# Kernel optimization log

Hardware: AMD Instinct MI355X
Metric: run time of the kernel (lower is better)

Reference implementation:

```python
import jax, jax.numpy as jnp
import numpy as np
from jax import lax

N, CIN, COUT, T, V, G, K = 32, 64, 64, 256, 25, 8, 3  # batch, channels, time, joints, groups, subsets
EPS = 1e-5  # BatchNorm eps


def setup_inputs() -> dict:
    key = jax.random.key(0)
    ks = jax.random.split(key, 10)
    x = jax.random.normal(ks[0], (N, CIN, T, V), jnp.float32)
    # DecoupleA param: A reshaped [3,1,V,V] tiled over groups (torch .repeat tiles)
    A0 = jax.random.uniform(ks[1], (K, 1, V, V), jnp.float32)
    DecoupleA = jnp.tile(A0, (1, G, 1, 1))
    W = jax.random.normal(ks[2], (CIN, COUT * K), jnp.float32) * np.float32(np.sqrt(0.5 / (COUT * K)))
    b = jnp.full((1, COUT * K, 1, 1), 1e-6, jnp.float32)
    g0 = 1.0 + 0.1 * jax.random.normal(ks[3], (COUT * K,), jnp.float32)
    b0 = 0.1 * jax.random.normal(ks[4], (COUT * K,), jnp.float32)
    g1 = 1.0 + 0.1 * jax.random.normal(ks[5], (COUT,), jnp.float32)
    b1 = 0.1 * jax.random.normal(ks[6], (COUT,), jnp.float32)
    conv_w = jax.random.normal(ks[7], (COUT, COUT, 9, 1), jnp.float32) * np.float32(np.sqrt(2.0 / (COUT * 9)))
    conv_b = jnp.zeros((COUT,), jnp.float32)
    g2 = 1.0 + 0.1 * jax.random.normal(ks[8], (COUT,), jnp.float32)
    b2 = 0.1 * jax.random.normal(ks[9], (COUT,), jnp.float32)
    return {"x": x, "DecoupleA": DecoupleA, "W": W, "b": b, "g0": g0, "b0": b0,
            "g1": g1, "b1": b1, "conv_w": conv_w, "conv_b": conv_b, "g2": g2, "b2": b2,
            "keep_prob": 1}


def _bn_eval(y, g, be):
    # inference BN with running_mean=0, running_var=1
    return y * (g / jnp.sqrt(1.0 + EPS))[None, :, None, None] + be[None, :, None, None]


def reference(x, DecoupleA, W, b, g0, b0, g1, b1, conv_w, conv_b, g2, b2, keep_prob):
    # ---- unit_gcn ----
    learn_A = jnp.tile(DecoupleA, (1, COUT // G, 1, 1))           # [3, COUT, V, V]
    # norm(): right-multiply by diag((colsum + 0.001)^-1) == scale columns
    invD = 1.0 / (jnp.sum(learn_A, axis=2) + 0.001)               # [3, COUT, V]
    normA = learn_A * invD[:, :, None, :]
    y = jnp.einsum('nctw,cd->ndtw', x, W) + b                     # [N, 3*COUT, T, V]
    y = _bn_eval(y, g0, b0)
    y = y.reshape(N, K, COUT, T, V)
    y = jnp.einsum('nkctv,kcvw->nctw', y, normA)                  # message passing
    y = _bn_eval(y, g1, b1)
    y = jax.nn.relu(y + x)                                        # down = identity (CIN==COUT)
    # ---- unit_tcn (keep_prob==1 -> DropBlocks are identity) ----
    z = lax.conv_general_dilated(y, conv_w, (1, 1), [(4, 4), (0, 0)],
                                 dimension_numbers=('NCHW', 'OIHW', 'NCHW'))
    z = z + conv_b[None, :, None, None]
    z = _bn_eval(z, g2, b2)
    # ---- residual (identity, CIN==COUT, stride=1; skip-DropBlocks identity) ----
    return jax.nn.relu(z + x)
```

## Files before the change

### kernel.cpp

```cpp
#include <hip/hip_runtime.h>
#include <hip/hip_bf16.h>
#include <stdint.h>


typedef const float* fp;
typedef __attribute__((ext_vector_type(8))) short short8;
typedef __attribute__((ext_vector_type(4))) float floatx4;

__device__ __forceinline__ float us2f(unsigned int u){
  union { unsigned int i; float f; } c; c.i = u << 16; return c.f;
}
__device__ __forceinline__ unsigned short f2us(float f){
  __hip_bfloat16 h = __float2bfloat16(f);
  return *reinterpret_cast<unsigned short*>(&h);
}
__device__ __forceinline__ void gload_lds16(const void* g, void* l){
  __builtin_amdgcn_global_load_lds(
      (const __attribute__((address_space(1))) void*)g,
      (__attribute__((address_space(3))) void*)l, 16, 0, 0);
}


__global__ __launch_bounds__(256) void k_prep(
    fp x, fp A, fp W, fp b, fp g0, fp b0, fp g1, fp b1,
    fp cw, fp cb, fp g2, fp b2,
    unsigned short* U, float* biasU, unsigned short* xb,
    float* cbe, unsigned short* cwetb)
{
  int bid = blockIdx.x, tid = threadIdx.x;
  const float inv_s = rsqrtf(1.0f + 1e-5f);
  __shared__ __align__(16) char smemraw[26624];

  if (bid < 1792) {
    int m = bid;
    if (m >= 1600) {
      for (int k = tid; k < 1600; k += 256) U[(long long)m*1600 + k] = 0;
      return;
    }
    float* nAL   = (float*)smemraw;
    float* WeffL = (float*)(smemraw + 512);
    float* cs3   = (float*)(smemraw + 1408);
    int c = m & 63, w = m >> 6, g = c & 7;
    if (tid < 75) {
      int kk = tid / 25, vv = tid % 25;
      nAL[tid] = A[((kk*8 + g)*25 + vv)*25 + w];
    }
    if (tid < 192) {
      int kk = tid >> 6, cin = tid & 63;
      WeffL[tid] = W[cin*192 + kk*64 + c] * (g0[kk*64 + c] * inv_s);
    }
    __syncthreads();
    if (tid < 3) {
      float s = 0.f;
      for (int vv = 0; vv < 25; vv++) s += nAL[tid*25 + vv];
      cs3[tid] = s + 0.001f;
    }
    __syncthreads();
    if (tid < 75) nAL[tid] = nAL[tid] / cs3[tid/25];
    __syncthreads();
    float s1 = g1[c] * inv_s;
    for (int k = tid; k < 1600; k += 256) {
      int cin = k / 25, vv = k - cin*25;
      float acc = WeffL[cin]       * nAL[vv]
                + WeffL[64 + cin]  * nAL[25 + vv]
                + WeffL[128 + cin] * nAL[50 + vv];
      acc *= s1;
      if (cin == c && vv == w) acc += 1.0f;
      U[(long long)m*1600 + k] = f2us(acc);
    }
    if (tid == 0) {
      float acc = 0.f;
      for (int kk = 0; kk < 3; kk++) {
        int d = kk*64 + c;
        float be = b[d] * (g0[d] * inv_s) + b0[d];
        for (int v = 0; v < 25; v++) acc += be * nAL[kk*25 + v];
      }
      biasU[m] = acc * s1 + b1[c];
    }
    return;
  }

  if (bid < 2816) {
    int bxt = bid - 1792;
    int n = bxt >> 5, tb = bxt & 31, t0 = tb*8;
    unsigned short* xs = (unsigned short*)smemraw;
    for (int e = tid; e < 12800; e += 256) {
      int c = e / 200, r = e - c*200, tt = r / 25, v = r - tt*25;
      xs[(c*8 + tt)*26 + v] = f2us(x[((n*64 + c)*256 + t0 + tt)*25 + v]);
    }
    __syncthreads();
    for (int e4 = tid; e4 < 3200; e4 += 256) {
      int base = e4 * 4;
      int tt = base / 1600, q0 = base - tt*1600;
      int c = q0 / 25, v = q0 - c*25;
      ushort4 pk;
      pk.x = xs[(c*8 + tt)*26 + v]; if (++v == 25){v = 0; c++;}
      pk.y = xs[(c*8 + tt)*26 + v]; if (++v == 25){v = 0; c++;}
      pk.z = xs[(c*8 + tt)*26 + v]; if (++v == 25){v = 0; c++;}
      pk.w = xs[(c*8 + tt)*26 + v];
      *(ushort4*)(xb + (long long)(n*256 + t0 + tt)*1600 + q0) = pk;
    }
    return;
  }

  int gid = (bid - 2816)*256 + tid;
  if (gid < 36864) {
    int o = gid / 576, r = gid % 576;
    int j = r / 64, i = r % 64;
    cwetb[gid] = f2us(cw[(o*64+i)*9 + j] * (g2[o] * inv_s));
    return;
  }
  gid -= 36864;
  if (gid < 64) {
    cbe[gid] = cb[gid] * (g2[gid] * inv_s) + b2[gid];
  }
}

__global__ __launch_bounds__(256, 2) void k_gemm(
    const unsigned short* U, const unsigned short* xb, const float* biasU,
    unsigned short* yb)
{
  int bm = blockIdx.x >> 6, bn = blockIdx.x & 63;
  int n = bn >> 1, t0 = (bn & 1) * 128;
  int tid = threadIdx.x, lane = tid & 63, wid = tid >> 6;
  int l15 = lane & 15, grp = lane >> 4;

  __shared__ __align__(16) unsigned short As[256*64];
  __shared__ __align__(16) unsigned short Bs[128*64];

  const unsigned short* gA[8];
  const unsigned short* gB[4];
  unsigned short* lA[8];
  unsigned short* lB[4];
  #pragma unroll
  for (int it = 0; it < 8; it++) {
    int e = it*256 + tid;
    int row = e >> 3, li = e & 7;
    int kcol = (li ^ (row & 7)) * 8;
    gA[it] = U + (long long)(bm*256 + row)*1600 + kcol;
    lA[it] = As + e*8;
  }
  #pragma unroll
  for (int it = 0; it < 4; it++) {
    int e = it*256 + tid;
    int row = e >> 3, li = e & 7;
    int kcol = (li ^ (row & 7)) * 8;
    gB[it] = xb + (long long)(n*256 + t0 + row)*1600 + kcol;
    lB[it] = Bs + e*8;
  }

  floatx4 acc[4][8];
  #pragma unroll
  for (int i = 0; i < 4; i++)
    #pragma unroll
    for (int j = 0; j < 8; j++) acc[i][j] = (floatx4){0.f,0.f,0.f,0.f};

  for (int kc = 0; kc < 25; kc++) {
    #pragma unroll
    for (int it = 0; it < 8; it++) gload_lds16(gA[it] + kc*64, lA[it]);
    #pragma unroll
    for (int it = 0; it < 4; it++) gload_lds16(gB[it] + kc*64, lB[it]);
    __syncthreads();
    #pragma unroll
    for (int ks = 0; ks < 2; ks++) {
      int colk = ((ks*4 + grp) ^ (l15 & 7)) * 8;
      short8 af[4], bf[8];
      #pragma unroll
      for (int i = 0; i < 4; i++)
        af[i] = *(const short8*)(As + (wid*64 + i*16 + l15)*64 + colk);
      #pragma unroll
      for (int j = 0; j < 8; j++)
        bf[j] = *(const short8*)(Bs + (j*16 + l15)*64 + colk);
      #pragma unroll
      for (int i = 0; i < 4; i++)
        #pragma unroll
        for (int j = 0; j < 8; j++)
          acc[i][j] = __builtin_amdgcn_mfma_f32_16x16x32_bf16(af[i], bf[j], acc[i][j], 0, 0, 0);
    }
    __syncthreads();
  }

  #pragma unroll
  for (int i = 0; i < 4; i++) {
    int mbase = bm*256 + wid*64 + i*16 + grp*4;
    if (mbase >= 1600) continue;
    float4 bu = *(const float4*)(biasU + mbase);
    #pragma unroll
    for (int j = 0; j < 8; j++) {
      int col = j*16 + l15;
      int t = t0 + col;
      ushort4 pk;
      pk.x = f2us(fmaxf(acc[i][j][0] + bu.x, 0.f));
      pk.y = f2us(fmaxf(acc[i][j][1] + bu.y, 0.f));
      pk.z = f2us(fmaxf(acc[i][j][2] + bu.z, 0.f));
      pk.w = f2us(fmaxf(acc[i][j][3] + bu.w, 0.f));
      *(ushort4*)(yb + (long long)(n*256 + t)*1600 + mbase) = pk;
    }
  }
}

__global__ __launch_bounds__(512) void k_tcn(
    const unsigned short* yb, const unsigned short* cwetb, const float* cbe,
    fp x, const unsigned short* zpg, float* out)
{
  int n = blockIdx.x >> 5, tb = blockIdx.x & 31, t0 = tb*8;
  int tid = threadIdx.x, lane = tid & 63, wid = tid >> 6;
  int l15 = lane & 15, grp = lane >> 4;
  __shared__ __align__(16) unsigned short ys[3584*8];

  #pragma unroll
  for (int it = 0; it < 7; it++) {
    int e = it*512 + tid;
    int row = e >> 3, li = e & 7;
    int rt = row / 25, v = row - rt*25;
    int tg = t0 - 4 + rt;
    int sli = li ^ (row & 7);
    bool ok = (row < 425) && (tg >= 0) && (tg < 256);
    const unsigned short* src = ok
      ? yb + ((long long)(n*256 + tg)*1600 + v*64 + sli*8)
      : zpg + li*8;
    gload_lds16(src, ys + e*8);
  }

  int p = wid & 3, h = wid >> 2;
  int o0 = p * 16;
  int o = o0 + l15;
  short8 af[9][2];
  #pragma unroll
  for (int j = 0; j < 9; j++) {
    af[j][0] = *(const short8*)(cwetb + ((o*9 + j)*64 + grp*8));
    af[j][1] = *(const short8*)(cwetb + ((o*9 + j)*64 + 32 + grp*8));
  }
  float4 cb4 = *(const float4*)(cbe + o0 + grp*4);
  __syncthreads();

  for (int tile = h; tile < 13; tile += 2) {
    int colb = tile*16 + l15;
    floatx4 acc = (floatx4){0.f,0.f,0.f,0.f};
    #pragma unroll
    for (int j = 0; j < 9; j++) {
      int row = colb + 25*j;
      int r7 = row & 7;
      const unsigned short* rb = ys + row*64;
      short8 b0 = *(const short8*)(rb + ((grp     ^ r7))*8);
      short8 b1 = *(const short8*)(rb + (((4+grp) ^ r7))*8);
      acc = __builtin_amdgcn_mfma_f32_16x16x32_bf16(af[j][0], b0, acc, 0, 0, 0);
      acc = __builtin_amdgcn_mfma_f32_16x16x32_bf16(af[j][1], b1, acc, 0, 0, 0);
    }
    if (colb < 200) {
      int tt = colb / 25, v = colb - tt*25, t = t0 + tt;
      #pragma unroll
      for (int r = 0; r < 4; r++) {
        int oo = o0 + grp*4 + r;
        float val = acc[r] + ((const float*)&cb4)[r]
                  + x[((n*64 + oo)*256 + t)*25 + v];
        out[((n*64 + oo)*256 + t)*25 + v] = fmaxf(val, 0.f);
      }
    }
  }
}

extern "C" void kernel_launch(void* const* d_in, const int* in_sizes, int n_in,
                              void* d_out, int out_size, void* d_ws, size_t ws_size,
                              hipStream_t stream)
{
  fp x  = (fp)d_in[0];
  fp A  = (fp)d_in[1];
  fp W  = (fp)d_in[2];
  fp b  = (fp)d_in[3];
  fp g0 = (fp)d_in[4];
  fp b0 = (fp)d_in[5];
  fp g1 = (fp)d_in[6];
  fp b1 = (fp)d_in[7];
  fp cw = (fp)d_in[8];
  fp cb = (fp)d_in[9];
  fp g2 = (fp)d_in[10];
  fp b2 = (fp)d_in[11];

  char* ws = (char*)d_ws;
  float*          cbe   = (float*)(ws + 117504);
  unsigned short* cwetb = (unsigned short*)(ws + 117760);
  float*          biasU = (float*)(ws + 191488);
  unsigned short* U     = (unsigned short*)(ws + 197888);
  unsigned short* xb    = (unsigned short*)(ws + 5932288);
  unsigned short* yb    = (unsigned short*)(ws + 32146688);
  const unsigned short* zpg = U + (long long)1600*1600;

  k_prep<<<2961, 256, 0, stream>>>(x, A, W, b, g0, b0, g1, b1, cw, cb, g2, b2,
                                   U, biasU, xb, cbe, cwetb);
  k_gemm<<<448, 256, 0, stream>>>(U, xb, biasU, yb);
  k_tcn<<<1024, 512, 0, stream>>>(yb, cwetb, cbe, x, zpg, (float*)d_out);
}
```

Before: 221.7 us.

## Swap MFMA operands for vectorized epilogue stores and split prep kernel

The TCN epilogue swaps the MFMA A/B operands so each lane holds four consecutive output positions for a single output channel. The residual read and the output write then become one float4 load and one nontemporal float4 store per lane, replacing four strided scalar accesses. The x-transpose part of the prep kernel is moved into its own kernel, so the U/weight prep blocks no longer reserve the large shared buffer. This adds an extra kernel launch in exchange for lower LDS usage and coalesced epilogue memory traffic.

Result: no change. 222.8 us (+0.5%).

```diff
diff --git a/kernel.cpp b/kernel.cpp
--- a/kernel.cpp
+++ b/kernel.cpp
@@ -21,15 +21,13 @@
 }
 
 
-__global__ __launch_bounds__(256) void k_prep(
-    fp x, fp A, fp W, fp b, fp g0, fp b0, fp g1, fp b1,
+__global__ __launch_bounds__(256) void k_prepU(
+    fp A, fp W, fp b, fp g0, fp b0, fp g1, fp b1,
     fp cw, fp cb, fp g2, fp b2,
-    unsigned short* U, float* biasU, unsigned short* xb,
-    float* cbe, unsigned short* cwetb)
+    unsigned short* U, float* biasU, float* cbe, unsigned short* cwetb)
 {
   int bid = blockIdx.x, tid = threadIdx.x;
   const float inv_s = rsqrtf(1.0f + 1e-5f);
-  __shared__ __align__(16) char smemraw[26624];
 
   if (bid < 1792) {
     int m = bid;
@@ -37,9 +35,9 @@
       for (int k = tid; k < 1600; k += 256) U[(long long)m*1600 + k] = 0;
       return;
     }
-    float* nAL   = (float*)smemraw;
-    float* WeffL = (float*)(smemraw + 512);
-    float* cs3   = (float*)(smemraw + 1408);
+    __shared__ float nAL[75];
+    __shared__ float WeffL[192];
+    __shared__ float cs3[3];
     int c = m & 63, w = m >> 6, g = c & 7;
     if (tid < 75) {
       int kk = tid / 25, vv = tid % 25;
@@ -80,30 +78,7 @@
     return;
   }
 
-  if (bid < 2816) {
-    int bxt = bid - 1792;
-    int n = bxt >> 5, tb = bxt & 31, t0 = tb*8;
-    unsigned short* xs = (unsigned short*)smemraw;
-    for (int e = tid; e < 12800; e += 256) {
-      int c = e / 200, r = e - c*200, tt = r / 25, v = r - tt*25;
-      xs[(c*8 + tt)*26 + v] = f2us(x[((n*64 + c)*256 + t0 + tt)*25 + v]);
-    }
-    __syncthreads();
-    for (int e4 = tid; e4 < 3200; e4 += 256) {
-      int base = e4 * 4;
-      int tt = base / 1600, q0 = base - tt*1600;
-      int c = q0 / 25, v = q0 - c*25;
-      ushort4 pk;
-      pk.x = xs[(c*8 + tt)*26 + v]; if (++v == 25){v = 0; c++;}
-      pk.y = xs[(c*8 + tt)*26 + v]; if (++v == 25){v = 0; c++;}
-      pk.z = xs[(c*8 + tt)*26 + v]; if (++v == 25){v = 0; c++;}
-      pk.w = xs[(c*8 + tt)*26 + v];
-      *(ushort4*)(xb + (long long)(n*256 + t0 + tt)*1600 + q0) = pk;
-    }
-    return;
-  }
-
-  int gid = (bid - 2816)*256 + tid;
+  int gid = (bid - 1792)*256 + tid;
   if (gid < 36864) {
     int o = gid / 576, r = gid % 576;
     int j = r / 64, i = r % 64;
@@ -113,6 +88,28 @@
   gid -= 36864;
   if (gid < 64) {
     cbe[gid] = cb[gid] * (g2[gid] * inv_s) + b2[gid];
+  }
+}
+
+__global__ __launch_bounds__(256) void k_xt(fp x, unsigned short* xb)
+{
+  int n = blockIdx.x >> 5, tb = blockIdx.x & 31, t0 = tb*8, tid = threadIdx.x;
+  __shared__ unsigned short xs[64*8*26];
+  for (int e = tid; e < 12800; e += 256) {
+    int c = e / 200, r = e - c*200, tt = r / 25, v = r - tt*25;
+    xs[(c*8 + tt)*26 + v] = f2us(x[((n*64 + c)*256 + t0 + tt)*25 + v]);
+  }
+  __syncthreads();
+  for (int e4 = tid; e4 < 3200; e4 += 256) {
+    int base = e4 * 4;
+    int tt = base / 1600, q0 = base - tt*1600;
+    int c = q0 / 25, v = q0 - c*25;
+    ushort4 pk;
+    pk.x = xs[(c*8 + tt)*26 + v]; if (++v == 25){v = 0; c++;}
+    pk.y = xs[(c*8 + tt)*26 + v]; if (++v == 25){v = 0; c++;}
+    pk.z = xs[(c*8 + tt)*26 + v]; if (++v == 25){v = 0; c++;}
+    pk.w = xs[(c*8 + tt)*26 + v];
+    *(ushort4*)(xb + (long long)(n*256 + t0 + tt)*1600 + q0) = pk;
   }
 }
 
@@ -231,7 +228,7 @@
     af[j][0] = *(const short8*)(cwetb + ((o*9 + j)*64 + grp*8));
     af[j][1] = *(const short8*)(cwetb + ((o*9 + j)*64 + 32 + grp*8));
   }
-  float4 cb4 = *(const float4*)(cbe + o0 + grp*4);
+  float cbv = cbe[o];
   __syncthreads();
 
   for (int tile = h; tile < 13; tile += 2) {
@@ -244,18 +241,19 @@
       const unsigned short* rb = ys + row*64;
       short8 b0 = *(const short8*)(rb + ((grp     ^ r7))*8);
       short8 b1 = *(const short8*)(rb + (((4+grp) ^ r7))*8);
-      acc = __builtin_amdgcn_mfma_f32_16x16x32_bf16(af[j][0], b0, acc, 0, 0, 0);
-      acc = __builtin_amdgcn_mfma_f32_16x16x32_bf16(af[j][1], b1, acc, 0, 0, 0);
-    }
-    if (colb < 200) {
-      int tt = colb / 25, v = colb - tt*25, t = t0 + tt;
-      #pragma unroll
-      for (int r = 0; r < 4; r++) {
-        int oo = o0 + grp*4 + r;
-        float val = acc[r] + ((const float*)&cb4)[r]
-                  + x[((n*64 + oo)*256 + t)*25 + v];
-        out[((n*64 + oo)*256 + t)*25 + v] = fmaxf(val, 0.f);
-      }
+      acc = __builtin_amdgcn_mfma_f32_16x16x32_bf16(b0, af[j][0], acc, 0, 0, 0);
+      acc = __builtin_amdgcn_mfma_f32_16x16x32_bf16(b1, af[j][1], acc, 0, 0, 0);
+    }
+    int colb0 = tile*16 + grp*4;
+    if (colb0 < 200) {
+      long long base = (long long)(n*64 + o)*6400 + t0*25 + colb0;
+      floatx4 xv = *(const floatx4*)(x + base);
+      floatx4 ov;
+      ov.x = fmaxf(acc.x + cbv + xv.x, 0.f);
+      ov.y = fmaxf(acc.y + cbv + xv.y, 0.f);
+      ov.z = fmaxf(acc.z + cbv + xv.z, 0.f);
+      ov.w = fmaxf(acc.w + cbv + xv.w, 0.f);
+      __builtin_nontemporal_store(ov, (floatx4*)(out + base));
     }
   }
 }
@@ -286,8 +284,9 @@
   unsigned short* yb    = (unsigned short*)(ws + 32146688);
   const unsigned short* zpg = U + (long long)1600*1600;
 
-  k_prep<<<2961, 256, 0, stream>>>(x, A, W, b, g0, b0, g1, b1, cw, cb, g2, b2,
-                                   U, biasU, xb, cbe, cwetb);
+  k_prepU<<<1937, 256, 0, stream>>>(A, W, b, g0, b0, g1, b1, cw, cb, g2, b2,
+                                    U, biasU, cbe, cwetb);
+  k_xt<<<1024, 256, 0, stream>>>(x, xb);
   k_gemm<<<448, 256, 0, stream>>>(U, xb, biasU, yb);
   k_tcn<<<1024, 512, 0, stream>>>(yb, cwetb, cbe, x, zpg, (float*)d_out);
 }
```
